# Performance work log

Hardware: AMD Instinct MI355X
Metric: run time of the kernel (lower is better)

## Reference

```python
import jax, jax.numpy as jnp
import numpy as np

HIDDEN = 2048
N_HEADS = 16
N_KV_HEADS = 4
HEAD_DIM = HIDDEN // N_HEADS  # 128
WINDOW = 2048
ROPE_THETA = 10000.0


def setup_inputs() -> dict:
    key = jax.random.key(0)
    ks = jax.random.split(key, 5)
    B, S = 1, 4096
    scale = 0.02
    return {
        "hidden_states": jax.random.normal(ks[0], (B, S, HIDDEN), dtype=jnp.float32),
        # nn.Linear weights are [out_features, in_features]
        "q_w": jax.random.normal(ks[1], (N_HEADS * HEAD_DIM, HIDDEN), dtype=jnp.float32) * scale,
        "k_w": jax.random.normal(ks[2], (N_KV_HEADS * HEAD_DIM, HIDDEN), dtype=jnp.float32) * scale,
        "v_w": jax.random.normal(ks[3], (N_KV_HEADS * HEAD_DIM, HIDDEN), dtype=jnp.float32) * scale,
        "o_w": jax.random.normal(ks[4], (HIDDEN, N_HEADS * HEAD_DIM), dtype=jnp.float32) * scale,
    }


def _rope_cos_sin(seq_len, dtype):
    inv_freq = 1.0 / (ROPE_THETA ** (jnp.arange(0, HEAD_DIM, 2, dtype=jnp.float32) / HEAD_DIM))
    pos = jnp.arange(seq_len, dtype=jnp.float32)
    freqs = pos[:, None] * inv_freq[None, :]          # [S, D/2]
    emb = jnp.concatenate([freqs, freqs], axis=-1)    # [S, D]
    return jnp.cos(emb).astype(dtype), jnp.sin(emb).astype(dtype)


def _rotate_half(x):
    x1, x2 = jnp.split(x, 2, axis=-1)
    return jnp.concatenate([-x2, x1], axis=-1)


def reference(hidden_states, q_w, k_w, v_w, o_w):
    B, S, _ = hidden_states.shape
    dtype = hidden_states.dtype

    q = hidden_states @ q_w.T                         # [B,S,H*D]
    k = hidden_states @ k_w.T                         # [B,S,Hkv*D]
    v = hidden_states @ v_w.T

    q = q.reshape(B, S, N_HEADS, HEAD_DIM).transpose(0, 2, 1, 3)      # [B,H,S,D]
    k = k.reshape(B, S, N_KV_HEADS, HEAD_DIM).transpose(0, 2, 1, 3)   # [B,Hkv,S,D]
    v = v.reshape(B, S, N_KV_HEADS, HEAD_DIM).transpose(0, 2, 1, 3)

    cos, sin = _rope_cos_sin(S, dtype)                # [S,D]
    cos = cos[None, None]
    sin = sin[None, None]
    q = q * cos + _rotate_half(q) * sin
    k = k * cos + _rotate_half(k) * sin

    n_rep = N_HEADS // N_KV_HEADS
    k = jnp.repeat(k, n_rep, axis=1)                  # [B,H,S,D]
    v = jnp.repeat(v, n_rep, axis=1)

    scores = jnp.einsum("bhqd,bhkd->bhqk", q, k) / jnp.sqrt(jnp.array(HEAD_DIM, dtype))

    pos = jnp.arange(S)
    rel = pos[:, None] - pos[None, :]
    allowed = (rel >= 0) & (rel < WINDOW)             # causal sliding window
    mask = jnp.where(allowed, jnp.array(0.0, dtype), jnp.array(-jnp.inf, dtype))
    scores = scores + mask[None, None]

    attn = jax.nn.softmax(scores.astype(jnp.float32), axis=-1).astype(dtype)

    out = jnp.einsum("bhqk,bhkd->bhqd", attn, v)      # [B,H,S,D]
    out = out.transpose(0, 2, 1, 3).reshape(B, S, N_HEADS * HEAD_DIM)
    return out @ o_w.T
```

## Files before the change

kernel.cpp:

```cpp
#include <hip/hip_runtime.h>
#include <stdint.h>

typedef unsigned short u16;
typedef unsigned int u32;
typedef float f32x4 __attribute__((ext_vector_type(4)));
typedef float f32x8 __attribute__((ext_vector_type(8)));
typedef int   i32x4 __attribute__((ext_vector_type(4)));
typedef __bf16 bf16x8 __attribute__((ext_vector_type(8)));
typedef u16 u16x4 __attribute__((ext_vector_type(4)));

constexpr int S_LEN = 4096;
constexpr int HID   = 2048;
constexpr int WIN   = 2048;

__device__ __forceinline__ u32 f2bf_u(float f) {
  u32 u = __builtin_bit_cast(u32, f);
  return (u + 0x7fffu + ((u >> 16) & 1u)) >> 16;
}
__device__ __forceinline__ float bf2f(u16 u) {
  return __builtin_bit_cast(float, ((u32)u) << 16);
}
__device__ __forceinline__ float exp2x(float x) {
#if __has_builtin(__builtin_amdgcn_exp2f)
  return __builtin_amdgcn_exp2f(x);
#else
  return exp2f(x);
#endif
}
__device__ __forceinline__ void mfma16(f32x4& acc, i32x4 a, i32x4 b) {
  acc = __builtin_amdgcn_mfma_f32_16x16x32_bf16(
      __builtin_bit_cast(bf16x8, a), __builtin_bit_cast(bf16x8, b), acc, 0, 0, 0);
}
__device__ __forceinline__ void gload_lds16(const u16* g, u16* l) {
  __builtin_amdgcn_global_load_lds((const __attribute__((address_space(1))) u32*)g,
                                   (__attribute__((address_space(3))) u32*)l, 16, 0, 0);
}

constexpr int CVT_B0 = 1048576;
constexpr int CVT_B1 = CVT_B0 + 524288;
constexpr int CVT_B2 = CVT_B1 + 131072;
constexpr int CVT_B3 = CVT_B2 + 131072;
constexpr int CVT_B4 = CVT_B3 + 524288;

__global__ __launch_bounds__(256) void cvt_all_kernel(
    const float* __restrict__ s0, const float* __restrict__ s1,
    const float* __restrict__ s2, const float* __restrict__ s3,
    const float* __restrict__ s4, u16* __restrict__ d0, u16* __restrict__ d1,
    u16* __restrict__ d2, u16* __restrict__ d3, u16* __restrict__ d4) {
  int t = blockIdx.x * 256 + threadIdx.x;
  const float* s;
  u16* d;
  int off;
  if (t < CVT_B0) { s = s0; d = d0; off = t; }
  else if (t < CVT_B1) { s = s1; d = d1; off = t - CVT_B0; }
  else if (t < CVT_B2) { s = s2; d = d2; off = t - CVT_B1; }
  else if (t < CVT_B3) { s = s3; d = d3; off = t - CVT_B2; }
  else { s = s4; d = d4; off = t - CVT_B3; }
  const f32x4* sp = (const f32x4*)s + (size_t)off * 2;
  f32x4 a = sp[0], b = sp[1];
  i32x4 o;
  o.x = (int)(f2bf_u(a.x) | (f2bf_u(a.y) << 16));
  o.y = (int)(f2bf_u(a.z) | (f2bf_u(a.w) << 16));
  o.z = (int)(f2bf_u(b.x) | (f2bf_u(b.y) << 16));
  o.w = (int)(f2bf_u(b.z) | (f2bf_u(b.w) << 16));
  *((i32x4*)d + off) = o;
}

__global__ __launch_bounds__(256) void rope_table_kernel(float* __restrict__ cs,
                                                         float* __restrict__ sn) {
  int t = blockIdx.x * 256 + threadIdx.x;
  int d = t & 63, s = t >> 6;
  float inv = exp2f(-(float)d * 0.20762050593046014f);
  float f = (float)s * inv;
  cs[t] = cosf(f);
  sn[t] = sinf(f);
}

__global__ __launch_bounds__(256) void qkv_gemm_kernel(
    const u16* __restrict__ A, const u16* __restrict__ Wq,
    const u16* __restrict__ Wk, const u16* __restrict__ Wv,
    u16* __restrict__ Qb, u16* __restrict__ Kb, u16* __restrict__ Vt,
    const float* __restrict__ cs, const float* __restrict__ sn) {
  __shared__ __attribute__((aligned(16))) u16 smem[128 * 128];
  u16* sA = smem;
  u16* sB = smem + 128 * 64;
  const int lane = threadIdx.x & 63;
  const int w = threadIdx.x >> 6;
  const int g = lane >> 4, ln = lane & 15;
  const int K = HID;

  int wgid = blockIdx.x;
  wgid = (wgid & 7) * 96 + (wgid >> 3);
  const int brow = (wgid / 24) * 128;
  const int bcol = (wgid % 24) * 128;

  const u16* B;
  u16* out;
  int bc, N;
  bool is_v = false;
  float rope_scale = 1.f;
  if (bcol < 2048) {
    B = Wq; out = Qb; bc = bcol; N = 2048;
    rope_scale = 0.088388347648318447f * 1.4426950408889634f;
  } else if (bcol < 2560) {
    B = Wk; out = Kb; bc = bcol - 2048; N = 512;
  } else {
    B = Wv; out = Vt; bc = bcol - 2560; N = 512; is_v = true;
  }

  const int wr = (w >> 1) * 64, wc = (w & 1) * 64;
  f32x4 acc[4][4] = {};

  const int sr = w * 32 + (lane >> 3);
  const int scol = (lane & 7) * 8;
  const u16* Abase = A + (size_t)(brow + sr) * K + scol;
  const u16* Bbase = B + (size_t)(bc + sr) * K + scol;
  u16* sAdst = &sA[w * 2048];
  u16* sBdst = &sB[w * 2048];

  for (int k0 = 0; k0 < K; k0 += 64) {
    __syncthreads();
#pragma unroll
    for (int i = 0; i < 4; ++i) {
      gload_lds16(Abase + (size_t)i * 8 * K + k0, sAdst + i * 512);
      gload_lds16(Bbase + (size_t)i * 8 * K + k0, sBdst + i * 512);
    }
    __syncthreads();
#pragma unroll
    for (int kk = 0; kk < 2; ++kk) {
      i32x4 af[4], bfr[4];
#pragma unroll
      for (int m = 0; m < 4; ++m)
        af[m] = *(const i32x4*)&sA[(wr + m * 16 + ln) * 64 + kk * 32 + g * 8];
#pragma unroll
      for (int n = 0; n < 4; ++n)
        bfr[n] = *(const i32x4*)&sB[(wc + n * 16 + ln) * 64 + kk * 32 + g * 8];
#pragma unroll
      for (int m = 0; m < 4; ++m)
#pragma unroll
        for (int n = 0; n < 4; ++n) mfma16(acc[m][n], af[m], bfr[n]);
    }
  }

  const int orow0 = brow + wr + g * 4;
  const int ocol0 = bc + wc + ln;

  if (is_v) {
#pragma unroll
    for (int m = 0; m < 4; ++m)
#pragma unroll
      for (int n = 0; n < 4; ++n)
#pragma unroll
        for (int j = 0; j < 4; ++j) {
          int row = orow0 + m * 16 + j;
          int col = ocol0 + n * 16;
          int d = col & 127, kvh = col >> 7;
          int T = row >> 5, ks = row & 31;
          int tt = ks >> 4, gg = (ks >> 2) & 3, e = (tt << 2) | (ks & 3);
          size_t idx = (size_t)kvh * S_LEN * 128 + (size_t)T * 4096 +
                       (size_t)d * 32 + ((size_t)(gg ^ ((d >> 1) & 3)) << 3) + e;
          out[idx] = (u16)f2bf_u(acc[m][n][j]);
        }
  } else {
    __syncthreads();
#pragma unroll
    for (int m = 0; m < 4; ++m)
#pragma unroll
      for (int n = 0; n < 4; ++n)
#pragma unroll
        for (int j = 0; j < 4; ++j)
          smem[(wr + m * 16 + g * 4 + j) * 128 + (wc + n * 16 + ln)] =
              (u16)f2bf_u(acc[m][n][j]);
    __syncthreads();
    const int r = threadIdx.x >> 1;
    const int half = threadIdx.x & 1;
    const int s = brow + r;
    u16* outp = out + (size_t)s * N + bc;
#pragma unroll
    for (int i = 0; i < 8; ++i) {
      const int d0 = half * 32 + i * 4;
      f32x4 c4 = *(const f32x4*)&cs[(s << 6) + d0];
      f32x4 s4 = *(const f32x4*)&sn[(s << 6) + d0];
      u16x4 a = *(const u16x4*)&smem[r * 128 + d0];
      u16x4 b = *(const u16x4*)&smem[r * 128 + d0 + 64];
      u16x4 oa, ob;
#pragma unroll
      for (int j = 0; j < 4; ++j) {
        float x1 = bf2f(a[j]), x2 = bf2f(b[j]);
        oa[j] = (u16)f2bf_u((x1 * c4[j] - x2 * s4[j]) * rope_scale);
        ob[j] = (u16)f2bf_u((x2 * c4[j] + x1 * s4[j]) * rope_scale);
      }
      *(u16x4*)(outp + d0) = oa;
      *(u16x4*)(outp + d0 + 64) = ob;
    }
  }
}

__global__ __launch_bounds__(256) void gemm_o_kernel(const u16* __restrict__ A,
                                                     const u16* __restrict__ B,
                                                     float* __restrict__ Cv,
                                                     int K, int N) {
  __shared__ __attribute__((aligned(16))) u16 sA[128 * 64];
  __shared__ __attribute__((aligned(16))) u16 sB[128 * 64];
  const int lane = threadIdx.x & 63;
  const int w = threadIdx.x >> 6;
  const int g = lane >> 4, ln = lane & 15;

  int wgid = blockIdx.y * gridDim.x + blockIdx.x;
  const int nwg = gridDim.x * gridDim.y;
  wgid = (wgid & 7) * (nwg >> 3) + (wgid >> 3);
  const int brow = (wgid / gridDim.x) * 128;
  const int bcol = (wgid % gridDim.x) * 128;
  const int wr = (w >> 1) * 64, wc = (w & 1) * 64;

  f32x4 acc[4][4] = {};

  const int sr = w * 32 + (lane >> 3);
  const int scol = (lane & 7) * 8;
  const u16* Abase = A + (size_t)(brow + sr) * K + scol;
  const u16* Bbase = B + (size_t)(bcol + sr) * K + scol;
  u16* sAdst = &sA[w * 2048];
  u16* sBdst = &sB[w * 2048];

  for (int k0 = 0; k0 < K; k0 += 64) {
    __syncthreads();
#pragma unroll
    for (int i = 0; i < 4; ++i) {
      gload_lds16(Abase + (size_t)i * 8 * K + k0, sAdst + i * 512);
      gload_lds16(Bbase + (size_t)i * 8 * K + k0, sBdst + i * 512);
    }
    __syncthreads();
#pragma unroll
    for (int kk = 0; kk < 2; ++kk) {
      i32x4 af[4], bfr[4];
#pragma unroll
      for (int m = 0; m < 4; ++m)
        af[m] = *(const i32x4*)&sA[(wr + m * 16 + ln) * 64 + kk * 32 + g * 8];
#pragma unroll
      for (int n = 0; n < 4; ++n)
        bfr[n] = *(const i32x4*)&sB[(wc + n * 16 + ln) * 64 + kk * 32 + g * 8];
#pragma unroll
      for (int m = 0; m < 4; ++m)
#pragma unroll
        for (int n = 0; n < 4; ++n) mfma16(acc[m][n], af[m], bfr[n]);
    }
  }

  const int orow0 = brow + wr + g * 4;
  const int ocol0 = bcol + wc + ln;
#pragma unroll
  for (int m = 0; m < 4; ++m)
#pragma unroll
    for (int n = 0; n < 4; ++n)
#pragma unroll
      for (int j = 0; j < 4; ++j)
        Cv[(size_t)(orow0 + m * 16 + j) * N + ocol0 + n * 16] = acc[m][n][j];
}

__global__ __launch_bounds__(64) void attn_kernel(const u16* __restrict__ Q,
                                                  const u16* __restrict__ Kb,
                                                  const u16* __restrict__ Vt,
                                                  u16* __restrict__ opart,
                                                  float* __restrict__ mpart,
                                                  float* __restrict__ lpart) {
  const int lane = threadIdx.x;
  const int g = lane >> 4, ln = lane & 15;

  const int o = blockIdx.x;
  const int r = o >> 3;
  const int h = ((o & 7) << 1) | ((r >> 1) & 1);
  const int chunk = r & 1;
  const int gq = 127 - (r >> 2);
  const int kvh = h >> 2;
  const int qr0 = gq * 32;

  i32x4 aq[2][4];
#pragma unroll
  for (int qf = 0; qf < 2; ++qf) {
    const u16* qp = Q + (size_t)(qr0 + qf * 16 + ln) * HID + h * 128 + g * 8;
#pragma unroll
    for (int c = 0; c < 4; ++c) aq[qf][c] = *(const i32x4*)(qp + c * 32);
  }

  f32x4 oacc[2][8] = {};
  float mrun[2] = {-1e30f, -1e30f};
  float lrun[2] = {0.f, 0.f};

  int lo = qr0 - (WIN - 1);
  if (lo < 0) lo = 0;
  lo &= ~31;
  const int nt_full = ((qr0 + 32) - lo) >> 5;
  const int nt0 = nt_full >> 1;
  const int lo_c = lo + (chunk ? nt0 * 32 : 0);
  const int nt = chunk ? nt_full - nt0 : nt0;

  const u16* kptr0 = Kb + (size_t)(lo_c + ln) * 512 + kvh * 128 + g * 8;
  const int vswz = (g ^ ((ln >> 1) & 3)) << 3;
  const u16* vptr0 = Vt + (size_t)kvh * S_LEN * 128 +
                     (size_t)(lo_c >> 5) * 4096 + ln * 32 + vswz;

  i32x4 kfA[2][4], kfB[2][4], vf[8];
  if (nt > 0) {
#pragma unroll
    for (int tt = 0; tt < 2; ++tt)
#pragma unroll
      for (int c = 0; c < 4; ++c)
        kfA[tt][c] = *(const i32x4*)(kptr0 + tt * 8192 + c * 32);
#pragma unroll
    for (int nf = 0; nf < 8; ++nf) vf[nf] = *(const i32x4*)(vptr0 + nf * 512);
  }
  if (nt > 1) {
#pragma unroll
    for (int tt = 0; tt < 2; ++tt)
#pragma unroll
      for (int c = 0; c < 4; ++c)
        kfB[tt][c] = *(const i32x4*)(kptr0 + 16384 + tt * 8192 + c * 32);
  }

#define TILE(T, KF)                                                            \
  {                                                                            \
    const int kb = lo_c + (T) * 32;                                            \
    f32x4 sc[2][2] = {};                                                       \
    __builtin_amdgcn_s_setprio(1);                                             \
    _Pragma("unroll") for (int c = 0; c < 4; ++c) {                            \
      mfma16(sc[0][0], KF[0][c], aq[0][c]);                                    \
      mfma16(sc[0][1], KF[1][c], aq[0][c]);                                    \
      mfma16(sc[1][0], KF[0][c], aq[1][c]);                                    \
      mfma16(sc[1][1], KF[1][c], aq[1][c]);                                    \
    }                                                                          \
    __builtin_amdgcn_s_setprio(0);                                             \
    if ((T) + 2 < nt) {             \
      const u16* kp = kptr0 + (size_t)((T) + 2) * 16384;                       \
      _Pragma("unroll") for (int tt = 0; tt < 2; ++tt)                         \
        _Pragma("unroll") for (int c = 0; c < 4; ++c)                          \
          KF[tt][c] = *(const i32x4*)(kp + tt * 8192 + c * 32);                \
    }                                                                          \
    float p[2][8], mx[2];                                                      \
    const bool interior = (kb + 31 <= qr0) && (qr0 + 31 - kb < WIN);           \
    _Pragma("unroll") for (int qf = 0; qf < 2; ++qf) {                         \
      if (interior) {                                                          \
        _Pragma("unroll") for (int j = 0; j < 4; ++j) {                        \
          p[qf][j] = sc[qf][0][j];                                             \
          p[qf][4 + j] = sc[qf][1][j];                                         \
        }                                                                      \
      } else {                                                                 \
        const float NEG = -__builtin_inff();                                   \
        const int q = qr0 + qf * 16 + ln;                                      \
        _Pragma("unroll") for (int tt = 0; tt < 2; ++tt)                       \
          _Pragma("unroll") for (int j = 0; j < 4; ++j) {                      \
            int k = kb + tt * 16 + g * 4 + j;                                  \
            p[qf][tt * 4 + j] = (k <= q && q - k < WIN) ? sc[qf][tt][j] : NEG; \
          }                                                                    \
      }                                                                        \
      float x0 = fmaxf(fmaxf(p[qf][0], p[qf][1]), p[qf][2]);                   \
      float x1 = fmaxf(fmaxf(p[qf][3], p[qf][4]), p[qf][5]);                   \
      float x2 = fmaxf(fmaxf(p[qf][6], p[qf][7]), x0);                         \
      float m = fmaxf(x1, x2);                                                 \
      m = fmaxf(m, __shfl_xor(m, 16));                                         \
      m = fmaxf(m, __shfl_xor(m, 32));                                         \
      mx[qf] = m;                                                              \
    }                                                                          \
    float corr[2] = {1.f, 1.f};                                                \
    const bool noskip =                                                        \
        !__all((mx[0] - mrun[0] <= 11.f) && (mx[1] - mrun[1] <= 11.f));        \
    if (noskip) {                                                              \
      _Pragma("unroll") for (int qf = 0; qf < 2; ++qf) {                       \
        float mnew = fmaxf(mrun[qf], mx[qf]);                                  \
        corr[qf] = exp2x(mrun[qf] - mnew);                                     \
        mrun[qf] = mnew;                                                       \
        f32x4 cv;                                                              \
        _Pragma("unroll") for (int j = 0; j < 4; ++j)                          \
            cv[j] = __shfl(corr[qf], g * 4 + j);                               \
        _Pragma("unroll") for (int nf = 0; nf < 8; ++nf)                       \
          _Pragma("unroll") for (int j = 0; j < 4; ++j)                        \
              oacc[qf][nf][j] *= cv[j];                                        \
      }                                                                        \
    }                                                                          \
    i32x4 pa[2];                                                               \
    _Pragma("unroll") for (int qf = 0; qf < 2; ++qf) {                         \
      f32x8 pv;                                                                \
      _Pragma("unroll") for (int e = 0; e < 8; ++e)                            \
          pv[e] = exp2x(p[qf][e] - mrun[qf]);                                  \
      float rs = ((pv[0] + pv[1]) + (pv[2] + pv[3])) +                         \
                 ((pv[4] + pv[5]) + (pv[6] + pv[7]));                          \
      lrun[qf] = lrun[qf] * corr[qf] + rs;                                     \
      bf16x8 pb = __builtin_convertvector(pv, bf16x8);                         \
      pa[qf] = __builtin_bit_cast(i32x4, pb);                                  \
    }                                                                          \
    __builtin_amdgcn_s_setprio(1);                                             \
    _Pragma("unroll") for (int nf = 0; nf < 8; ++nf) {                         \
      mfma16(oacc[0][nf], pa[0], vf[nf]);                                      \
      mfma16(oacc[1][nf], pa[1], vf[nf]);                                      \
    }                                                                          \
    __builtin_amdgcn_s_setprio(0);                                             \
    if ((T) + 1 < nt) {                           \
      const u16* vp = vptr0 + (size_t)((T) + 1) * 4096;                        \
      _Pragma("unroll") for (int nf = 0; nf < 8; ++nf)                         \
          vf[nf] = *(const i32x4*)(vp + nf * 512);                             \
    }                                                                          \
  }

  int t = 0;
  for (; t + 1 < nt; t += 2) {
    TILE(t, kfA);
    TILE(t + 1, kfB);
  }
  if (t < nt) TILE(t, kfA);
#undef TILE

#pragma unroll
  for (int qf = 0; qf < 2; ++qf) {
    float l = lrun[qf];
    l += __shfl_xor(l, 16);
    l += __shfl_xor(l, 32);
    lrun[qf] = l;
  }

  const size_t pb = ((size_t)chunk * 16 + h) * S_LEN;
#pragma unroll
  for (int qf = 0; qf < 2; ++qf) {
    if (g == 0) {
      mpart[pb + qr0 + qf * 16 + ln] = mrun[qf];
      lpart[pb + qr0 + qf * 16 + ln] = lrun[qf];
    }
    u16* aop = opart + (pb + qr0 + qf * 16 + g * 4) * 128 + ln;
#pragma unroll
    for (int j = 0; j < 4; ++j)
#pragma unroll
      for (int nf = 0; nf < 8; ++nf)
        aop[(size_t)j * 128 + nf * 16] = (u16)f2bf_u(oacc[qf][nf][j]);
  }
}

__global__ __launch_bounds__(256) void attn_combine_kernel(
    const u16* __restrict__ opart, const float* __restrict__ mpart,
    const float* __restrict__ lpart, u16* __restrict__ AO) {
  int t = blockIdx.x * 256 + threadIdx.x;
  int d0 = (t & 15) * 8;
  int rh = t >> 4;
  int row = rh & (S_LEN - 1);
  int h = rh >> 12;
  size_t i0 = (size_t)h * S_LEN + row;
  size_t i1 = i0 + (size_t)16 * S_LEN;
  float m0 = mpart[i0], m1 = mpart[i1];
  float l0 = lpart[i0], l1 = lpart[i1];
  float m = fmaxf(m0, m1);
  float w0 = exp2x(m0 - m), w1 = exp2x(m1 - m);
  float inv = 1.f / (l0 * w0 + l1 * w1);
  w0 *= inv;
  w1 *= inv;
  i32x4 v0 = *(const i32x4*)(opart + i0 * 128 + d0);
  i32x4 v1 = *(const i32x4*)(opart + i1 * 128 + d0);
  i32x4 ov;
#pragma unroll
  for (int j = 0; j < 4; ++j) {
    u32 a = ((u32)v0[j]), b = ((u32)v1[j]);
    float x = bf2f((u16)a) * w0 + bf2f((u16)b) * w1;
    float y = bf2f((u16)(a >> 16)) * w0 + bf2f((u16)(b >> 16)) * w1;
    ov[j] = (int)(f2bf_u(x) | (f2bf_u(y) << 16));
  }
  *(i32x4*)(AO + (size_t)row * HID + h * 128 + d0) = ov;
}

extern "C" void kernel_launch(void* const* d_in, const int* in_sizes, int n_in,
                              void* d_out, int out_size, void* d_ws, size_t ws_size,
                              hipStream_t stream) {
  const float* hx = (const float*)d_in[0];
  const float* qw = (const float*)d_in[1];
  const float* kw = (const float*)d_in[2];
  const float* vw = (const float*)d_in[3];
  const float* ow = (const float*)d_in[4];

  char* p = (char*)d_ws;
  u16* Xb = (u16*)p; p += (size_t)S_LEN * HID * 2;
  u16* Wq = (u16*)p; p += (size_t)HID * HID * 2;
  u16* Wk = (u16*)p; p += (size_t)512 * HID * 2;
  u16* Wv = (u16*)p; p += (size_t)512 * HID * 2;
  u16* Wo = (u16*)p; p += (size_t)HID * HID * 2;
  u16* Qb = (u16*)p; p += (size_t)S_LEN * HID * 2;
  u16* Kb = (u16*)p; p += (size_t)S_LEN * 512 * 2;
  u16* Vt = (u16*)p; p += (size_t)S_LEN * 512 * 2;
  u16* AO = (u16*)p; p += (size_t)S_LEN * HID * 2;
  float* cs = (float*)p; p += (size_t)S_LEN * 64 * 4;
  float* sn = (float*)p; p += (size_t)S_LEN * 64 * 4;
  u16* Opart = (u16*)p; p += (size_t)2 * 16 * S_LEN * 128 * 2;
  float* Mpart = (float*)p; p += (size_t)2 * 16 * S_LEN * 4;
  float* Lpart = (float*)p; p += (size_t)2 * 16 * S_LEN * 4;

  cvt_all_kernel<<<CVT_B4 / 256, 256, 0, stream>>>(hx, qw, kw, vw, ow, Xb, Wq,
                                                   Wk, Wv, Wo);
  rope_table_kernel<<<S_LEN * 64 / 256, 256, 0, stream>>>(cs, sn);

  qkv_gemm_kernel<<<768, 256, 0, stream>>>(Xb, Wq, Wk, Wv, Qb, Kb, Vt, cs, sn);

  attn_kernel<<<4096, 64, 0, stream>>>(Qb, Kb, Vt, Opart, Mpart, Lpart);
  attn_combine_kernel<<<S_LEN * 16 * 16 / 256, 256, 0, stream>>>(Opart, Mpart,
                                                                 Lpart, AO);

  gemm_o_kernel<<<dim3(16, 32), 256, 0, stream>>>(AO, Wo, (float*)d_out, HID,
                                                  HID);
}
```

Baseline: 333.0 us.

## Software-pipeline QK^T one tile ahead in attention; move RoPE into separate kernel

The attention loop now computes the score MFMAs for tile T+1 before running softmax and PV for tile T. Two score buffers alternate, so the matrix work can overlap the exp and reduction work of the previous tile, at the cost of more registers. Separately, RoPE is taken out of the QKV GEMM epilogue and done in a standalone elementwise kernel. This simplifies the GEMM epilogue (no LDS staging or extra syncs) but adds a launch and a read-modify-write pass over Q and K.

```diff
diff --git a/kernel.cpp b/kernel.cpp
--- a/kernel.cpp
+++ b/kernel.cpp
@@ -76,14 +76,47 @@
   sn[t] = sinf(f);
 }
 
+__global__ __launch_bounds__(256) void rope_qk_kernel(u16* __restrict__ Qb,
+                                                      u16* __restrict__ Kb,
+                                                      const float* __restrict__ cs,
+                                                      const float* __restrict__ sn) {
+  const float SC2 = 0.088388347648318447f * 1.4426950408889634f;
+  int t = blockIdx.x * 256 + threadIdx.x;
+  int d0 = (t & 15) * 4;
+  int r = t >> 4;
+  u16* p;
+  int s;
+  float qs;
+  if (r < S_LEN * 16) {
+    int h = r & 15; s = r >> 4;
+    p = Qb + (size_t)s * HID + h * 128 + d0;
+    qs = SC2;
+  } else {
+    int r2 = r - S_LEN * 16;
+    int h = r2 & 3; s = r2 >> 2;
+    p = Kb + (size_t)s * 512 + h * 128 + d0;
+    qs = 1.f;
+  }
+  f32x4 c = *(const f32x4*)&cs[(s << 6) | d0];
+  f32x4 si = *(const f32x4*)&sn[(s << 6) | d0];
+  u16x4 a = *(u16x4*)p, b = *(u16x4*)(p + 64);
+  u16x4 oa, ob;
+#pragma unroll
+  for (int j = 0; j < 4; ++j) {
+    float x1 = bf2f(a[j]), x2 = bf2f(b[j]);
+    oa[j] = (u16)f2bf_u((x1 * c[j] - x2 * si[j]) * qs);
+    ob[j] = (u16)f2bf_u((x2 * c[j] + x1 * si[j]) * qs);
+  }
+  *(u16x4*)p = oa;
+  *(u16x4*)(p + 64) = ob;
+}
+
 __global__ __launch_bounds__(256) void qkv_gemm_kernel(
     const u16* __restrict__ A, const u16* __restrict__ Wq,
     const u16* __restrict__ Wk, const u16* __restrict__ Wv,
-    u16* __restrict__ Qb, u16* __restrict__ Kb, u16* __restrict__ Vt,
-    const float* __restrict__ cs, const float* __restrict__ sn) {
-  __shared__ __attribute__((aligned(16))) u16 smem[128 * 128];
-  u16* sA = smem;
-  u16* sB = smem + 128 * 64;
+    u16* __restrict__ Qb, u16* __restrict__ Kb, u16* __restrict__ Vt) {
+  __shared__ __attribute__((aligned(16))) u16 sA[128 * 64];
+  __shared__ __attribute__((aligned(16))) u16 sB[128 * 64];
   const int lane = threadIdx.x & 63;
   const int w = threadIdx.x >> 6;
   const int g = lane >> 4, ln = lane & 15;
@@ -96,17 +129,10 @@
 
   const u16* B;
   u16* out;
-  int bc, N;
-  bool is_v = false;
-  float rope_scale = 1.f;
-  if (bcol < 2048) {
-    B = Wq; out = Qb; bc = bcol; N = 2048;
-    rope_scale = 0.088388347648318447f * 1.4426950408889634f;
-  } else if (bcol < 2560) {
-    B = Wk; out = Kb; bc = bcol - 2048; N = 512;
-  } else {
-    B = Wv; out = Vt; bc = bcol - 2560; N = 512; is_v = true;
-  }
+  int bc, mode, N;
+  if (bcol < 2048)      { B = Wq; out = Qb; bc = bcol;        N = 2048; mode = 0; }
+  else if (bcol < 2560) { B = Wk; out = Kb; bc = bcol - 2048; N = 512;  mode = 0; }
+  else                  { B = Wv; out = Vt; bc = bcol - 2560; N = 512;  mode = 1; }
 
   const int wr = (w >> 1) * 64, wc = (w & 1) * 64;
   f32x4 acc[4][4] = {};
@@ -144,56 +170,26 @@
 
   const int orow0 = brow + wr + g * 4;
   const int ocol0 = bc + wc + ln;
-
-  if (is_v) {
-#pragma unroll
-    for (int m = 0; m < 4; ++m)
-#pragma unroll
-      for (int n = 0; n < 4; ++n)
-#pragma unroll
-        for (int j = 0; j < 4; ++j) {
-          int row = orow0 + m * 16 + j;
-          int col = ocol0 + n * 16;
+#pragma unroll
+  for (int m = 0; m < 4; ++m)
+#pragma unroll
+    for (int n = 0; n < 4; ++n)
+#pragma unroll
+      for (int j = 0; j < 4; ++j) {
+        int row = orow0 + m * 16 + j;
+        int col = ocol0 + n * 16;
+        float v = acc[m][n][j];
+        if (mode == 0) {
+          out[(size_t)row * N + col] = (u16)f2bf_u(v);
+        } else {
           int d = col & 127, kvh = col >> 7;
           int T = row >> 5, ks = row & 31;
           int tt = ks >> 4, gg = (ks >> 2) & 3, e = (tt << 2) | (ks & 3);
           size_t idx = (size_t)kvh * S_LEN * 128 + (size_t)T * 4096 +
                        (size_t)d * 32 + ((size_t)(gg ^ ((d >> 1) & 3)) << 3) + e;
-          out[idx] = (u16)f2bf_u(acc[m][n][j]);
+          out[idx] = (u16)f2bf_u(v);
         }
-  } else {
-    __syncthreads();
-#pragma unroll
-    for (int m = 0; m < 4; ++m)
-#pragma unroll
-      for (int n = 0; n < 4; ++n)
-#pragma unroll
-        for (int j = 0; j < 4; ++j)
-          smem[(wr + m * 16 + g * 4 + j) * 128 + (wc + n * 16 + ln)] =
-              (u16)f2bf_u(acc[m][n][j]);
-    __syncthreads();
-    const int r = threadIdx.x >> 1;
-    const int half = threadIdx.x & 1;
-    const int s = brow + r;
-    u16* outp = out + (size_t)s * N + bc;
-#pragma unroll
-    for (int i = 0; i < 8; ++i) {
-      const int d0 = half * 32 + i * 4;
-      f32x4 c4 = *(const f32x4*)&cs[(s << 6) + d0];
-      f32x4 s4 = *(const f32x4*)&sn[(s << 6) + d0];
-      u16x4 a = *(const u16x4*)&smem[r * 128 + d0];
-      u16x4 b = *(const u16x4*)&smem[r * 128 + d0 + 64];
-      u16x4 oa, ob;
-#pragma unroll
-      for (int j = 0; j < 4; ++j) {
-        float x1 = bf2f(a[j]), x2 = bf2f(b[j]);
-        oa[j] = (u16)f2bf_u((x1 * c4[j] - x2 * s4[j]) * rope_scale);
-        ob[j] = (u16)f2bf_u((x2 * c4[j] + x1 * s4[j]) * rope_scale);
       }
-      *(u16x4*)(outp + d0) = oa;
-      *(u16x4*)(outp + d0 + 64) = ob;
-    }
-  }
 }
 
 __global__ __launch_bounds__(256) void gemm_o_kernel(const u16* __restrict__ A,
@@ -299,49 +295,39 @@
   const u16* vptr0 = Vt + (size_t)kvh * S_LEN * 128 +
                      (size_t)(lo_c >> 5) * 4096 + ln * 32 + vswz;
 
-  i32x4 kfA[2][4], kfB[2][4], vf[8];
-  if (nt > 0) {
-#pragma unroll
-    for (int tt = 0; tt < 2; ++tt)
-#pragma unroll
-      for (int c = 0; c < 4; ++c)
-        kfA[tt][c] = *(const i32x4*)(kptr0 + tt * 8192 + c * 32);
-#pragma unroll
-    for (int nf = 0; nf < 8; ++nf) vf[nf] = *(const i32x4*)(vptr0 + nf * 512);
-  }
-  if (nt > 1) {
-#pragma unroll
-    for (int tt = 0; tt < 2; ++tt)
-#pragma unroll
-      for (int c = 0; c < 4; ++c)
-        kfB[tt][c] = *(const i32x4*)(kptr0 + 16384 + tt * 8192 + c * 32);
-  }
-
-#define TILE(T, KF)                                                            \
+  i32x4 kfN[2][4], vf[8];
+  f32x4 scA[2][2], scB[2][2];
+
+#define TILE_P(T, SCC, SCN)                                                    \
   {                                                                            \
     const int kb = lo_c + (T) * 32;                                            \
-    f32x4 sc[2][2] = {};                                                       \
-    __builtin_amdgcn_s_setprio(1);                                             \
-    _Pragma("unroll") for (int c = 0; c < 4; ++c) {                            \
-      mfma16(sc[0][0], KF[0][c], aq[0][c]);                                    \
-      mfma16(sc[0][1], KF[1][c], aq[0][c]);                                    \
-      mfma16(sc[1][0], KF[0][c], aq[1][c]);                                    \
-      mfma16(sc[1][1], KF[1][c], aq[1][c]);                                    \
-    }                                                                          \
-    __builtin_amdgcn_s_setprio(0);                                             \
-    if ((T) + 2 < nt) {             \
-      const u16* kp = kptr0 + (size_t)((T) + 2) * 16384;                       \
-      _Pragma("unroll") for (int tt = 0; tt < 2; ++tt)                         \
-        _Pragma("unroll") for (int c = 0; c < 4; ++c)                          \
-          KF[tt][c] = *(const i32x4*)(kp + tt * 8192 + c * 32);                \
+    if ((T) + 1 < nt) { \
+      SCN[0][0] = (f32x4){};                                                   \
+      SCN[0][1] = (f32x4){};                                                   \
+      SCN[1][0] = (f32x4){};                                                   \
+      SCN[1][1] = (f32x4){};                                                   \
+      __builtin_amdgcn_s_setprio(1);                                           \
+      _Pragma("unroll") for (int c = 0; c < 4; ++c) {                          \
+        mfma16(SCN[0][0], kfN[0][c], aq[0][c]);                                \
+        mfma16(SCN[0][1], kfN[1][c], aq[0][c]);                                \
+        mfma16(SCN[1][0], kfN[0][c], aq[1][c]);                                \
+        mfma16(SCN[1][1], kfN[1][c], aq[1][c]);                                \
+      }                                                                        \
+      __builtin_amdgcn_s_setprio(0);                                           \
+      if ((T) + 2 < nt) {                          \
+        const u16* kp = kptr0 + (size_t)((T) + 2) * 16384;                     \
+        _Pragma("unroll") for (int tt = 0; tt < 2; ++tt)                       \
+          _Pragma("unroll") for (int c = 0; c < 4; ++c)                        \
+            kfN[tt][c] = *(const i32x4*)(kp + tt * 8192 + c * 32);             \
+      }                                                                        \
     }                                                                          \
     float p[2][8], mx[2];                                                      \
     const bool interior = (kb + 31 <= qr0) && (qr0 + 31 - kb < WIN);           \
     _Pragma("unroll") for (int qf = 0; qf < 2; ++qf) {                         \
       if (interior) {                                                          \
         _Pragma("unroll") for (int j = 0; j < 4; ++j) {                        \
-          p[qf][j] = sc[qf][0][j];                                             \
-          p[qf][4 + j] = sc[qf][1][j];                                         \
+          p[qf][j] = SCC[qf][0][j];                                            \
+          p[qf][4 + j] = SCC[qf][1][j];                                        \
         }                                                                      \
       } else {                                                                 \
         const float NEG = -__builtin_inff();                                   \
@@ -349,7 +335,7 @@
         _Pragma("unroll") for (int tt = 0; tt < 2; ++tt)                       \
           _Pragma("unroll") for (int j = 0; j < 4; ++j) {                      \
             int k = kb + tt * 16 + g * 4 + j;                                  \
-            p[qf][tt * 4 + j] = (k <= q && q - k < WIN) ? sc[qf][tt][j] : NEG; \
+            p[qf][tt * 4 + j] = (k <= q && q - k < WIN) ? SCC[qf][tt][j] : NEG;\
           }                                                                    \
       }                                                                        \
       float x0 = fmaxf(fmaxf(p[qf][0], p[qf][1]), p[qf][2]);                   \
@@ -393,20 +379,51 @@
       mfma16(oacc[1][nf], pa[1], vf[nf]);                                      \
     }                                                                          \
     __builtin_amdgcn_s_setprio(0);                                             \
-    if ((T) + 1 < nt) {                           \
+    if ((T) + 1 < nt) {                             \
       const u16* vp = vptr0 + (size_t)((T) + 1) * 4096;                        \
       _Pragma("unroll") for (int nf = 0; nf < 8; ++nf)                         \
           vf[nf] = *(const i32x4*)(vp + nf * 512);                             \
     }                                                                          \
   }
 
-  int t = 0;
-  for (; t + 1 < nt; t += 2) {
-    TILE(t, kfA);
-    TILE(t + 1, kfB);
-  }
-  if (t < nt) TILE(t, kfA);
-#undef TILE
+  if (nt > 0) {
+#pragma unroll
+    for (int tt = 0; tt < 2; ++tt)
+#pragma unroll
+      for (int c = 0; c < 4; ++c)
+        kfN[tt][c] = *(const i32x4*)(kptr0 + tt * 8192 + c * 32);
+#pragma unroll
+    for (int nf = 0; nf < 8; ++nf) vf[nf] = *(const i32x4*)(vptr0 + nf * 512);
+    scA[0][0] = (f32x4){};
+    scA[0][1] = (f32x4){};
+    scA[1][0] = (f32x4){};
+    scA[1][1] = (f32x4){};
+    __builtin_amdgcn_s_setprio(1);
+#pragma unroll
+    for (int c = 0; c < 4; ++c) {
+      mfma16(scA[0][0], kfN[0][c], aq[0][c]);
+      mfma16(scA[0][1], kfN[1][c], aq[0][c]);
+      mfma16(scA[1][0], kfN[0][c], aq[1][c]);
+      mfma16(scA[1][1], kfN[1][c], aq[1][c]);
+    }
+    __builtin_amdgcn_s_setprio(0);
+    if (1 < nt) {
+      const u16* kp = kptr0 + 16384;
+#pragma unroll
+      for (int tt = 0; tt < 2; ++tt)
+#pragma unroll
+        for (int c = 0; c < 4; ++c)
+          kfN[tt][c] = *(const i32x4*)(kp + tt * 8192 + c * 32);
+    }
+
+    int t = 0;
+    for (; t + 1 < nt; t += 2) {
+      TILE_P(t, scA, scB);
+      TILE_P(t + 1, scB, scA);
+    }
+    if (t < nt) TILE_P(t, scA, scB);
+  }
+#undef TILE_P
 
 #pragma unroll
   for (int qf = 0; qf < 2; ++qf) {
@@ -491,7 +508,9 @@
                                                    Wk, Wv, Wo);
   rope_table_kernel<<<S_LEN * 64 / 256, 256, 0, stream>>>(cs, sn);
 
-  qkv_gemm_kernel<<<768, 256, 0, stream>>>(Xb, Wq, Wk, Wv, Qb, Kb, Vt, cs, sn);
+  qkv_gemm_kernel<<<768, 256, 0, stream>>>(Xb, Wq, Wk, Wv, Qb, Kb, Vt);
+
+  rope_qk_kernel<<<S_LEN * 20 * 16 / 256, 256, 0, stream>>>(Qb, Kb, cs, sn);
 
   attn_kernel<<<4096, 64, 0, stream>>>(Qb, Kb, Vt, Opart, Mpart, Lpart);
   attn_combine_kernel<<<S_LEN * 16 * 16 / 256, 256, 0, stream>>>(Opart, Mpart,
```

Result: faster. 318.4 us (-4.4%).
